# Kernel tuning notes

Measured on AMD Instinct MI355X. Metric: run time of the kernel, lower is better.

The kernel has to match this reference:

```python
import jax, jax.numpy as jnp
import numpy as np

B, S, E = 8, 2048, 512
VOCAB, FVOCAB = 32000, 128
SCALE = float(np.power(E, 0.5))  # emb_size ** (0.5 * temper), temper=1


def setup_inputs() -> dict:
    key = jax.random.key(0)
    ks = jax.random.split(key, 7)
    key_seq = jax.random.randint(ks[0], (B, S), 0, VOCAB, dtype=jnp.int32)
    value_seq = jax.random.randint(ks[1], (B, S), 0, FVOCAB, dtype=jnp.int32)
    hidden = jax.random.normal(ks[2], (B, S, E), dtype=jnp.float32)
    mask_matrix = jax.random.uniform(ks[3], (B, S, S), dtype=jnp.float32)
    nan_matrix = jnp.zeros((1,), dtype=jnp.int32)  # unused by forward
    # learned params; padding_idx=0 -> zero row in embeddings
    key_emb = jax.random.normal(ks[4], (VOCAB, E), dtype=jnp.float32).at[0].set(0.0)
    value_emb = jax.random.normal(ks[5], (FVOCAB, E), dtype=jnp.float32).at[0].set(0.0)
    weight = jax.random.normal(ks[6], (E, E), dtype=jnp.float32) / np.sqrt(E)
    return {
        "key_seq": key_seq, "value_seq": value_seq, "hidden": hidden,
        "mask_matrix": mask_matrix, "nan_matrix": nan_matrix,
        "key_emb": key_emb, "value_emb": value_emb, "weight": weight,
    }


def reference(key_seq, value_seq, hidden, mask_matrix, nan_matrix,
              key_emb, value_emb, weight):
    k = key_emb[key_seq]          # [B,S,E]
    v = value_emb[value_seq]      # [B,S,E]
    q = jnp.einsum('bsd,de->bse', hidden, weight)   # hidden @ weight
    u = jnp.einsum('bse,bte->bst', q, k) / SCALE    # QK^T, [B,S,S]
    mask = jnp.clip(mask_matrix.astype(u.dtype), 0.0, 1.0)
    exp_u = jnp.exp(u)
    delta = exp_u * mask
    p = delta / (jnp.sum(delta, axis=2, keepdims=True) + 1e-10)
    o = jnp.einsum('bst,bte->bse', p, v)            # PV, [B,S,E]
    return o
```

## Files before the change

### kernel.cpp

```cpp
#include <hip/hip_runtime.h>
#include <stdint.h>

#define BB 8
#define SS 2048
#define EE 512
#define INV_SCALE 0.04419417382415922f

typedef __attribute__((ext_vector_type(8))) short bf8_t;
typedef __attribute__((ext_vector_type(4))) float f4_t;

__device__ __forceinline__ unsigned short f2bf(float f) {
    union { float f; uint32_t u; } x; x.f = f;
    uint32_t r = x.u + 0x7fffu + ((x.u >> 16) & 1u);
    return (unsigned short)(r >> 16);
}


__global__ void __launch_bounds__(256) gather_k_kernel(const int* __restrict__ idx,
                                                       const float* __restrict__ emb,
                                                       unsigned short* __restrict__ out) {
    int id = blockIdx.x * 256 + threadIdx.x;
    int chunk = id & 63;
    int row = id >> 6;
    int e0 = chunk * 8;
    int k = idx[row];
    const float* src = emb + (size_t)k * EE + e0;
    float4 a = *(const float4*)(src);
    float4 c = *(const float4*)(src + 4);
    union { unsigned short s[8]; int4 v; } u;
    u.s[0] = f2bf(a.x); u.s[1] = f2bf(a.y); u.s[2] = f2bf(a.z); u.s[3] = f2bf(a.w);
    u.s[4] = f2bf(c.x); u.s[5] = f2bf(c.y); u.s[6] = f2bf(c.z); u.s[7] = f2bf(c.w);
    *(int4*)(out + (size_t)row * EE + e0) = u.v;
}

__global__ void __launch_bounds__(256) cast_h_kernel(const float* __restrict__ in,
                                                     unsigned short* __restrict__ out) {
    int id = blockIdx.x * 256 + threadIdx.x;
    const float* src = in + (size_t)id * 8;
    float4 a = *(const float4*)(src);
    float4 c = *(const float4*)(src + 4);
    union { unsigned short s[8]; int4 v; } u;
    u.s[0] = f2bf(a.x); u.s[1] = f2bf(a.y); u.s[2] = f2bf(a.z); u.s[3] = f2bf(a.w);
    u.s[4] = f2bf(c.x); u.s[5] = f2bf(c.y); u.s[6] = f2bf(c.z); u.s[7] = f2bf(c.w);
    *(int4*)(out + (size_t)id * 8) = u.v;
}

__global__ void __launch_bounds__(256) gather_vt_kernel(const int* __restrict__ idx,
                                                        const float* __restrict__ emb,
                                                        unsigned short* __restrict__ vt) {
    int id = blockIdx.x * 256 + threadIdx.x;
    int t = id & (SS - 1);
    int rest = id >> 11;
    int e = rest & (EE - 1);
    int b = rest >> 9;
    int k = idx[b * SS + t];
    vt[id] = f2bf(emb[(size_t)k * EE + e]);
}

__global__ void __launch_bounds__(256) transpose_w_kernel(const float* __restrict__ w,
                                                          unsigned short* __restrict__ wt) {
    int id = blockIdx.x * 256 + threadIdx.x;
    int e = id & (EE - 1);
    int f = id >> 9;
    wt[id] = f2bf(w[(size_t)e * EE + f] * INV_SCALE);
}


__device__ __forceinline__ void stage_tile(const unsigned short* gbase, int ld, int k0,
                                           unsigned short* lds, int wave, int lane) {
#pragma unroll
    for (int i = 0; i < 2; ++i) {
        int row = i * 64 + wave * 16 + (lane >> 2);
        int col = (lane & 3) * 8;
        const unsigned short* g = gbase + (size_t)row * ld + (k0 + col);
        unsigned short* l = lds + i * 2048 + wave * 512 + lane * 8;
        __builtin_amdgcn_global_load_lds((const __attribute__((address_space(1))) unsigned int*)g,
                                         (__attribute__((address_space(3))) unsigned int*)l,
                                         16, 0, 0);
    }
}

template <int KLEN>
__device__ __forceinline__ void mfma_loop(const unsigned short* Abase, int lda,
                                          const unsigned short* Bbase, int ldb,
                                          unsigned short* As, unsigned short* Bs,
                                          f4_t acc[4][4], int wave, int lane) {
    const int wm = wave >> 1, wn = wave & 1;
    const int quad = lane >> 4, l16 = lane & 15;
#pragma unroll 1
    for (int k0 = 0; k0 < KLEN; k0 += 32) {
        stage_tile(Abase, lda, k0, As, wave, lane);
        stage_tile(Bbase, ldb, k0, Bs, wave, lane);
        __syncthreads();
        bf8_t af[4], bfr[4];
#pragma unroll
        for (int mi = 0; mi < 4; ++mi)
            af[mi] = *(const bf8_t*)(As + (wm * 64 + mi * 16 + l16) * 32 + quad * 8);
#pragma unroll
        for (int ni = 0; ni < 4; ++ni)
            bfr[ni] = *(const bf8_t*)(Bs + (wn * 64 + ni * 16 + l16) * 32 + quad * 8);
#pragma unroll
        for (int mi = 0; mi < 4; ++mi)
#pragma unroll
            for (int ni = 0; ni < 4; ++ni)
                acc[mi][ni] = __builtin_amdgcn_mfma_f32_16x16x32_bf16(af[mi], bfr[ni],
                                                                      acc[mi][ni], 0, 0, 0);
        __syncthreads();
    }
}


__global__ void __launch_bounds__(256) qgen_kernel(const unsigned short* __restrict__ H,
                                                   const unsigned short* __restrict__ Wt,
                                                   unsigned short* __restrict__ Q) {
    __shared__ unsigned short As[128 * 32];
    __shared__ unsigned short Bs[128 * 32];
    const int tid = threadIdx.x, wave = tid >> 6, lane = tid & 63;
    const int rowT = blockIdx.y;
    const int colT = blockIdx.x;
    f4_t acc[4][4];
    const f4_t z = {0.f, 0.f, 0.f, 0.f};
    for (int i = 0; i < 4; ++i) for (int j = 0; j < 4; ++j) acc[i][j] = z;
    mfma_loop<EE>(H + (size_t)rowT * 128 * EE, EE,
                  Wt + (size_t)colT * 128 * EE, EE, As, Bs, acc, wave, lane);
    const int wm = wave >> 1, wn = wave & 1, quad = lane >> 4, l16 = lane & 15;
#pragma unroll
    for (int mi = 0; mi < 4; ++mi)
#pragma unroll
        for (int r = 0; r < 4; ++r) {
            int row = rowT * 128 + wm * 64 + mi * 16 + quad * 4 + r;
#pragma unroll
            for (int ni = 0; ni < 4; ++ni) {
                int col = colT * 128 + wn * 64 + ni * 16 + l16;
                Q[(size_t)row * EE + col] = f2bf(acc[mi][ni][r]);
            }
        }
}

__global__ void __launch_bounds__(256) qk_kernel(const unsigned short* __restrict__ Q,
                                                 const unsigned short* __restrict__ K,
                                                 const float* __restrict__ mask,
                                                 unsigned short* __restrict__ delta,
                                                 float* __restrict__ lsum) {
    __shared__ unsigned short As[128 * 32];
    __shared__ unsigned short Bs[128 * 32];
    const int tid = threadIdx.x, wave = tid >> 6, lane = tid & 63;
    const int b = blockIdx.z, qT = blockIdx.y, tT = blockIdx.x;
    f4_t acc[4][4];
    const f4_t z = {0.f, 0.f, 0.f, 0.f};
    for (int i = 0; i < 4; ++i) for (int j = 0; j < 4; ++j) acc[i][j] = z;
    mfma_loop<EE>(Q + ((size_t)b * SS + qT * 128) * EE, EE,
                  K + ((size_t)b * SS + tT * 128) * EE, EE, As, Bs, acc, wave, lane);
    const int wm = wave >> 1, wn = wave & 1, quad = lane >> 4, l16 = lane & 15;
#pragma unroll
    for (int mi = 0; mi < 4; ++mi)
#pragma unroll
        for (int r = 0; r < 4; ++r) {
            int row = qT * 128 + wm * 64 + mi * 16 + quad * 4 + r;
            const float* mrow = mask + ((size_t)b * SS + row) * SS;
            unsigned short* drow = delta + ((size_t)b * SS + row) * SS;
            float psum = 0.f;
#pragma unroll
            for (int ni = 0; ni < 4; ++ni) {
                int col = tT * 128 + wn * 64 + ni * 16 + l16;
                float m = mrow[col];
                m = fminf(fmaxf(m, 0.f), 1.f);
                float e = __expf(acc[mi][ni][r]) * m;
                drow[col] = f2bf(e);
                psum += e;
            }
#pragma unroll
            for (int off = 1; off < 16; off <<= 1)
                psum += __shfl_xor(psum, off, 16);
            if (l16 == 0) atomicAdd(&lsum[b * SS + row], psum);
        }
}

__global__ void __launch_bounds__(256) pv_kernel(const unsigned short* __restrict__ delta,
                                                 const unsigned short* __restrict__ Vt,
                                                 const float* __restrict__ lsum,
                                                 float* __restrict__ out) {
    __shared__ unsigned short As[128 * 32];
    __shared__ unsigned short Bs[128 * 32];
    const int tid = threadIdx.x, wave = tid >> 6, lane = tid & 63;
    const int b = blockIdx.z, qT = blockIdx.y, eT = blockIdx.x;
    f4_t acc[4][4];
    const f4_t z = {0.f, 0.f, 0.f, 0.f};
    for (int i = 0; i < 4; ++i) for (int j = 0; j < 4; ++j) acc[i][j] = z;
    mfma_loop<SS>(delta + ((size_t)b * SS + qT * 128) * SS, SS,
                  Vt + ((size_t)b * EE + eT * 128) * SS, SS, As, Bs, acc, wave, lane);
    const int wm = wave >> 1, wn = wave & 1, quad = lane >> 4, l16 = lane & 15;
#pragma unroll
    for (int mi = 0; mi < 4; ++mi)
#pragma unroll
        for (int r = 0; r < 4; ++r) {
            int row = qT * 128 + wm * 64 + mi * 16 + quad * 4 + r;
            float inv = 1.0f / (lsum[b * SS + row] + 1e-10f);
#pragma unroll
            for (int ni = 0; ni < 4; ++ni) {
                int col = eT * 128 + wn * 64 + ni * 16 + l16;
                out[((size_t)b * SS + row) * EE + col] = acc[mi][ni][r] * inv;
            }
        }
}


extern "C" void kernel_launch(void* const* d_in, const int* in_sizes, int n_in,
                              void* d_out, int out_size, void* d_ws, size_t ws_size,
                              hipStream_t stream) {
    const int*   key_seq = (const int*)d_in[0];
    const int*   val_seq = (const int*)d_in[1];
    const float* hidden  = (const float*)d_in[2];
    const float* mask    = (const float*)d_in[3];
    const float* key_emb = (const float*)d_in[5];
    const float* val_emb = (const float*)d_in[6];
    const float* weight  = (const float*)d_in[7];
    float* out = (float*)d_out;

    char* ws = (char*)d_ws;
    const size_t SZ_BSE = (size_t)BB * SS * EE * sizeof(unsigned short);
    unsigned short* Q    = (unsigned short*)(ws);
    unsigned short* K    = (unsigned short*)(ws + SZ_BSE);
    unsigned short* Vt   = (unsigned short*)(ws + 2 * SZ_BSE);
    unsigned short* H    = (unsigned short*)(ws + 3 * SZ_BSE);
    unsigned short* Wt   = (unsigned short*)(ws + 4 * SZ_BSE);
    float*          lsum = (float*)(ws + 4 * SZ_BSE + 524288);
    unsigned short* delta= (unsigned short*)(ws + 4 * SZ_BSE + 524288 + 65536);

    hipMemsetAsync(lsum, 0, (size_t)BB * SS * sizeof(float), stream);

    gather_k_kernel<<<4096, 256, 0, stream>>>(key_seq, key_emb, K);
    cast_h_kernel<<<4096, 256, 0, stream>>>(hidden, H);
    gather_vt_kernel<<<32768, 256, 0, stream>>>(val_seq, val_emb, Vt);
    transpose_w_kernel<<<1024, 256, 0, stream>>>(weight, Wt);

    qgen_kernel<<<dim3(4, 128), 256, 0, stream>>>(H, Wt, Q);
    qk_kernel<<<dim3(16, 16, 8), 256, 0, stream>>>(Q, K, mask, delta, lsum);
    pv_kernel<<<dim3(4, 16, 8), 256, 0, stream>>>(delta, Vt, lsum, out);
}
```

Measured before the change: 447.3 us.

## Double-buffer LDS tiles and XOR-swizzle chunks to avoid bank conflicts

Result: faster. 436.4 us (-2.4%).

```diff
diff --git a/kernel.cpp b/kernel.cpp
--- a/kernel.cpp
+++ b/kernel.cpp
@@ -68,11 +68,11 @@
 
 __device__ __forceinline__ void stage_tile(const unsigned short* gbase, int ld, int k0,
                                            unsigned short* lds, int wave, int lane) {
+    const int srcchunk = ((lane & 3) ^ ((lane >> 3) & 3)) * 8;
 #pragma unroll
     for (int i = 0; i < 2; ++i) {
         int row = i * 64 + wave * 16 + (lane >> 2);
-        int col = (lane & 3) * 8;
-        const unsigned short* g = gbase + (size_t)row * ld + (k0 + col);
+        const unsigned short* g = gbase + (size_t)row * ld + k0 + srcchunk;
         unsigned short* l = lds + i * 2048 + wave * 512 + lane * 8;
         __builtin_amdgcn_global_load_lds((const __attribute__((address_space(1))) unsigned int*)g,
                                          (__attribute__((address_space(3))) unsigned int*)l,
@@ -85,20 +85,30 @@
                                           const unsigned short* Bbase, int ldb,
                                           unsigned short* As, unsigned short* Bs,
                                           f4_t acc[4][4], int wave, int lane) {
-    const int wm = wave >> 1, wn = wave & 1;
-    const int quad = lane >> 4, l16 = lane & 15;
+    const int wm = wave >> 1, wn = wave & 1, quad = lane >> 4, l16 = lane & 15;
+    const int qs = (quad ^ ((l16 >> 1) & 3)) * 8;
+    constexpr int NT = KLEN / 32;
+
+    stage_tile(Abase, lda, 0, As, wave, lane);
+    stage_tile(Bbase, ldb, 0, Bs, wave, lane);
+    __syncthreads();
+
+    int cur = 0;
 #pragma unroll 1
-    for (int k0 = 0; k0 < KLEN; k0 += 32) {
-        stage_tile(Abase, lda, k0, As, wave, lane);
-        stage_tile(Bbase, ldb, k0, Bs, wave, lane);
-        __syncthreads();
+    for (int t = 0; t < NT; ++t) {
+        if (t + 1 < NT) {
+            stage_tile(Abase, lda, (t + 1) * 32, As + ((cur ^ 1) << 12), wave, lane);
+            stage_tile(Bbase, ldb, (t + 1) * 32, Bs + ((cur ^ 1) << 12), wave, lane);
+        }
+        const unsigned short* a = As + (cur << 12);
+        const unsigned short* b = Bs + (cur << 12);
         bf8_t af[4], bfr[4];
 #pragma unroll
         for (int mi = 0; mi < 4; ++mi)
-            af[mi] = *(const bf8_t*)(As + (wm * 64 + mi * 16 + l16) * 32 + quad * 8);
+            af[mi] = *(const bf8_t*)(a + (wm * 64 + mi * 16 + l16) * 32 + qs);
 #pragma unroll
         for (int ni = 0; ni < 4; ++ni)
-            bfr[ni] = *(const bf8_t*)(Bs + (wn * 64 + ni * 16 + l16) * 32 + quad * 8);
+            bfr[ni] = *(const bf8_t*)(b + (wn * 64 + ni * 16 + l16) * 32 + qs);
 #pragma unroll
         for (int mi = 0; mi < 4; ++mi)
 #pragma unroll
@@ -106,6 +116,7 @@
                 acc[mi][ni] = __builtin_amdgcn_mfma_f32_16x16x32_bf16(af[mi], bfr[ni],
                                                                       acc[mi][ni], 0, 0, 0);
         __syncthreads();
+        cur ^= 1;
     }
 }
 
@@ -113,8 +124,8 @@
 __global__ void __launch_bounds__(256) qgen_kernel(const unsigned short* __restrict__ H,
                                                    const unsigned short* __restrict__ Wt,
                                                    unsigned short* __restrict__ Q) {
-    __shared__ unsigned short As[128 * 32];
-    __shared__ unsigned short Bs[128 * 32];
+    __shared__ unsigned short As[2 * 128 * 32];
+    __shared__ unsigned short Bs[2 * 128 * 32];
     const int tid = threadIdx.x, wave = tid >> 6, lane = tid & 63;
     const int rowT = blockIdx.y;
     const int colT = blockIdx.x;
@@ -142,8 +153,8 @@
                                                  const float* __restrict__ mask,
                                                  unsigned short* __restrict__ delta,
                                                  float* __restrict__ lsum) {
-    __shared__ unsigned short As[128 * 32];
-    __shared__ unsigned short Bs[128 * 32];
+    __shared__ unsigned short As[2 * 128 * 32];
+    __shared__ unsigned short Bs[2 * 128 * 32];
     const int tid = threadIdx.x, wave = tid >> 6, lane = tid & 63;
     const int b = blockIdx.z, qT = blockIdx.y, tT = blockIdx.x;
     f4_t acc[4][4];
@@ -180,8 +191,8 @@
                                                  const unsigned short* __restrict__ Vt,
                                                  const float* __restrict__ lsum,
                                                  float* __restrict__ out) {
-    __shared__ unsigned short As[128 * 32];
-    __shared__ unsigned short Bs[128 * 32];
+    __shared__ unsigned short As[2 * 128 * 32];
+    __shared__ unsigned short Bs[2 * 128 * 32];
     const int tid = threadIdx.x, wave = tid >> 6, lane = tid & 63;
     const int b = blockIdx.z, qT = blockIdx.y, eT = blockIdx.x;
     f4_t acc[4][4];
```
